# Performance work log

Measured on AMD Instinct MI355X. Metric: run time of the kernel, lower is better.

Reference implementation:

```python
import jax, jax.numpy as jnp
import numpy as np
import itertools

# ---- module constants (mirroring HyperLayer init) ----
B = 16          # batchsize
K = 16384       # number of learned index tuples (k)
ADD = 32        # additional sampled integer tuples per point
RANK = 2        # len(learn_cols) = w_rank; learn_cols = (0, 1)
P = 2 ** RANK + ADD  # candidate integer tuples per real-valued point
IN_DIM = 65536
OUT_DIM = 65536
EPSILON = 1e-6
SIGMA_BOOST = 2.0

# floor/ceil mask: rows of itertools.product([True, False], repeat=RANK) -> (2^RANK, RANK)
_FLOOR_MASK = jnp.array(
    [[int(b) for b in bools] for bools in itertools.product([True, False], repeat=RANK)],
    dtype=bool,
)


def setup_inputs() -> dict:
    key = jax.random.key(0)
    k1, k2, k3, k4 = jax.random.split(key, 4)
    return {
        "x": jax.random.normal(k1, (B, IN_DIM), jnp.float32),
        "res": jax.random.normal(k2, (B, K, RANK + 2), jnp.float32),
        "bias": jax.random.normal(k3, (OUT_DIM,), jnp.float32),
        "temp_indices": jax.random.randint(k4, (K, 2), 0, IN_DIM, dtype=jnp.int64),
    }


def _forward(x, res, bias, temp_indices):
    bsz = x.shape[0]
    # subrange = [out_size, in_size] for learn_cols = (0, 1)
    size = jnp.array([OUT_DIM, IN_DIM], jnp.float32)

    # ---- split_out: means in [0, size-1], sigmas softplus-scaled by size ----
    means = jax.nn.sigmoid(res[..., :RANK]) * (size - 1.0)               # (B, K, 2)
    sigmas = (jax.nn.softplus(res[..., RANK] + SIGMA_BOOST) + EPSILON)[..., None] * size  # (B, K, 2)
    values = res[..., RANK + 1]                                          # (B, K)

    # ---- discretize: 2^RANK floor/ceil neighbors (on detached means) ----
    m_det = jax.lax.stop_gradient(means)[:, :, None, :]                  # (B, K, 1, 2)
    nb = jnp.where(_FLOOR_MASK[None, None], jnp.floor(m_det), jnp.ceil(m_det)).astype(jnp.int32)  # (B,K,4,2)

    # additional uniformly sampled integer tuples (fixed internal key, deterministic)
    u = jax.random.uniform(jax.random.key(42), (bsz, K, ADD, RANK), jnp.float32) * (1.0 - EPSILON)
    samp = jnp.floor(u * size).astype(jnp.int32)                         # (B, K, ADD, 2)

    ints = jnp.concatenate([nb, samp], axis=2)                           # (B, K, P, 2)
    ints_fl = ints.astype(jnp.float32)

    # diagonal-Gaussian densities of integer tuples under (means, sigmas)
    z = (ints_fl - means[:, :, None, :]) / sigmas[:, :, None, :]         # (B, K, P, 2)
    props = jnp.exp(-0.5 * jnp.sum(z * z, axis=-1))                      # (B, K, P)
    props = props / jnp.sum(props + EPSILON, axis=2, keepdims=True)

    vals = (values[:, :, None] * props).reshape(bsz, -1)                 # (B, L)
    idx = ints.reshape(bsz, -1, RANK)                                    # (B, L, 2)

    # template: hardwired temp_indices, with learn_cols overwritten by discretized indices
    template = jnp.broadcast_to(
        temp_indices.astype(jnp.int32)[None, :, None, :], (bsz, K, P, 2)
    ).reshape(bsz, -1, 2)
    template = template.at[:, :, jnp.array([0, 1])].set(idx)

    out_idx = template[..., 0]                                           # (B, L) in [0, OUT_DIM)
    in_idx = template[..., 1]                                            # (B, L) in [0, IN_DIM)

    # sparse matrix-vector product per batch element: gather then scatter-add
    gathered = jnp.take_along_axis(x, in_idx, axis=1)                    # (B, L)
    contrib = vals * gathered                                            # (B, L)
    flat = (jnp.arange(bsz, dtype=jnp.int32)[:, None] * OUT_DIM + out_idx).reshape(-1)
    y = jnp.zeros((bsz * OUT_DIM,), x.dtype).at[flat].add(contrib.reshape(-1))
    return y.reshape(bsz, OUT_DIM) + bias[None, :]


def reference(x, res, bias, temp_indices):
    return _forward(x, res, bias, temp_indices)
```

## Files before the change

kernel.cpp:

```cpp
#include <hip/hip_runtime.h>
#include <stdint.h>
#include <math.h>

#define NB 16
#define NK 16384
#define NADD 32
#define NP 36
#define DIM 65536
#define NCH 4
#define CHW 16384
#define GPB 16

__device__ __forceinline__ uint32_t rotl32(uint32_t x, uint32_t r) {
    return (x << r) | (x >> (32u - r));
}

__device__ __forceinline__ uint32_t tf_bits(uint32_t idx) {
    const uint32_t K1 = 42u;
    const uint32_t K2 = 0x1BD11BDAu ^ 42u;
    uint32_t x0 = 0u;
    uint32_t x1 = idx + K1;
#define TF_ROUND(r) { x0 += x1; x1 = rotl32(x1, r); x1 ^= x0; }
#define TF_G(a,b,c,d) TF_ROUND(a) TF_ROUND(b) TF_ROUND(c) TF_ROUND(d)
    TF_G(13,15,26,6)   x0 += K1;  x1 += K2 + 1u;
    TF_G(17,29,16,24)  x0 += K2;  x1 += 2u;
    TF_G(13,15,26,6)              x1 += K1 + 3u;
    TF_G(17,29,16,24)  x0 += K1;  x1 += K2 + 4u;
    TF_G(13,15,26,6)   x0 += K2;  x1 += 5u;
#undef TF_G
#undef TF_ROUND
    return x0 ^ x1;
}

__device__ __forceinline__ float xla_expf(float x0) {
    float x = fminf(fmaxf(x0, -88.3762626647949f), 88.3762626647950f);
    const float fx = floorf(__fadd_rn(__fmul_rn(x, 1.44269504088896341f), 0.5f));
    const float tmp = __fmul_rn(fx, 0.693359375f);
    float z = __fmul_rn(fx, -2.12194440e-4f);
    float r = __fsub_rn(x, tmp);
    r = __fsub_rn(r, z);
    z = __fmul_rn(r, r);
    float y = 1.9875691500E-4f;
    y = __fadd_rn(__fmul_rn(y, r), 1.3981999507E-3f);
    y = __fadd_rn(__fmul_rn(y, r), 8.3334519073E-3f);
    y = __fadd_rn(__fmul_rn(y, r), 4.1665795894E-2f);
    y = __fadd_rn(__fmul_rn(y, r), 1.6666665459E-1f);
    y = __fadd_rn(__fmul_rn(y, r), 5.0000001201E-1f);
    y = __fadd_rn(__fmul_rn(y, z), r);
    y = __fadd_rn(y, 1.0f);
    const int n = (int)fx;
    const float p2n = __uint_as_float((uint32_t)(n + 127) << 23);
    return fmaxf(__fmul_rn(y, p2n), x0);
}

__device__ __forceinline__ void gen_point(const float4 r, uint32_t tid,
                                          uint32_t* packed, float* w) {
    const float e0 = xla_expf(-r.x);
    const float e1 = xla_expf(-r.y);
    const float s0 = __fdiv_rn(1.0f, __fadd_rn(1.0f, e0));
    const float s1 = __fdiv_rn(1.0f, __fadd_rn(1.0f, e1));
    const float m0 = __fmul_rn(s0, 65535.0f);
    const float m1 = __fmul_rn(s1, 65535.0f);

    const float a2 = r.z + 2.0f;
    const float sp = fmaxf(a2, 0.0f) + log1pf(expf(-fabsf(a2)));
    const float sigma = (sp + 1e-6f) * 65536.0f;
    const float val = r.w;

    const float f0 = floorf(m0), c0 = ceilf(m0);
    const float f1 = floorf(m1), c1 = ceilf(m1);
    {
        const float cd0[4] = {f0, f0, c0, c0};
        const float cd1[4] = {f1, c1, f1, c1};
        #pragma unroll
        for (int p = 0; p < 4; ++p) {
            const float z0 = (cd0[p] - m0) / sigma;
            const float z1 = (cd1[p] - m1) / sigma;
            w[p] = expf(-0.5f * (z0*z0 + z1*z1));
            packed[p] = ((uint32_t)(int)cd0[p] << 16) | (uint32_t)(int)cd1[p];
        }
    }
    const float ONE_MEPS = (float)(1.0 - 1e-6);
    const uint32_t base = tid * 64u;
    #pragma unroll
    for (int a = 0; a < NADD; ++a) {
        const uint32_t bb0 = tf_bits(base + 2u*(uint32_t)a);
        const uint32_t bb1 = tf_bits(base + 2u*(uint32_t)a + 1u);
        const float u0 = __fmul_rn(__uint_as_float((bb0 >> 9) | 0x3f800000u) - 1.0f, ONE_MEPS);
        const float u1 = __fmul_rn(__uint_as_float((bb1 >> 9) | 0x3f800000u) - 1.0f, ONE_MEPS);
        const float s0f = floorf(__fmul_rn(u0, 65536.0f));
        const float s1f = floorf(__fmul_rn(u1, 65536.0f));
        const float z0 = (s0f - m0) / sigma;
        const float z1 = (s1f - m1) / sigma;
        w[4 + a] = expf(-0.5f * (z0*z0 + z1*z1));
        packed[4 + a] = ((uint32_t)(int)s0f << 16) | (uint32_t)(int)s1f;
    }
    float denom = 0.0f;
    #pragma unroll
    for (int p = 0; p < NP; ++p) denom += w[p] + 1e-6f;
    const float scale = val / denom;
    #pragma unroll
    for (int p = 0; p < NP; ++p) w[p] *= scale;
}


__global__ __launch_bounds__(1024) void f1_gen_reduce(
    const float*  __restrict__ x,
    const float4* __restrict__ res4,
    float* __restrict__ part)
{
    __shared__ float acc[CHW];
    const int blk = blockIdx.x;
    const int b = blk >> 4;
    const uint32_t tid = (uint32_t)blk * 1024u + threadIdx.x;

    uint32_t packed[NP];
    float    w[NP];
    gen_point(res4[tid], tid, packed, w);

    const float* __restrict__ xrow = x + ((size_t)b << 16);
    #pragma unroll
    for (int p = 0; p < NP; ++p) w[p] *= xrow[packed[p] & 0xFFFFu];

    float* __restrict__ dst = part + ((size_t)blk << 16);
    #pragma unroll 1
    for (int c = 0; c < NCH; ++c) {
        for (int j = threadIdx.x; j < CHW; j += 1024) acc[j] = 0.0f;
        __syncthreads();
        #pragma unroll
        for (int p = 0; p < NP; ++p) {
            if ((packed[p] >> 30) == (uint32_t)c)
                atomicAdd(&acc[(packed[p] >> 16) & (CHW - 1)], w[p]);
        }
        __syncthreads();
        for (int j = threadIdx.x; j < CHW; j += 1024) dst[c * CHW + j] = acc[j];
        __syncthreads();
    }
}

__global__ __launch_bounds__(256) void f2_final(
    const float4* __restrict__ part4,
    const float4* __restrict__ bias4,
    float4* __restrict__ y4)
{
    const int i = blockIdx.x * 256 + threadIdx.x;
    const int o4 = i & 16383;
    const int b = i >> 14;
    float4 s = bias4[o4];
    #pragma unroll
    for (int g = 0; g < GPB; ++g) {
        const float4 p = part4[(((size_t)(b * GPB + g)) << 14) + o4];
        s.x += p.x; s.y += p.y; s.z += p.z; s.w += p.w;
    }
    y4[i] = s;
}


__global__ __launch_bounds__(256) void init_bias_kernel(
    const float4* __restrict__ bias4, float4* __restrict__ y4)
{
    const int i = blockIdx.x * 256 + threadIdx.x;
    y4[i] = bias4[i & 16383];
}

__global__ __launch_bounds__(256) void hyper_scatter(
    const float*  __restrict__ x,
    const float4* __restrict__ res4,
    float*        __restrict__ y)
{
    const int tid = blockIdx.x * 256 + threadIdx.x;
    const int b = tid >> 14;
    uint32_t packed[NP];
    float    w[NP];
    gen_point(res4[tid], (uint32_t)tid, packed, w);
    const float* __restrict__ xrow = x + ((size_t)b << 16);
    float*       __restrict__ yrow = y + ((size_t)b << 16);
    #pragma unroll
    for (int p = 0; p < NP; ++p) {
        const float xv = xrow[packed[p] & 0xFFFFu];
        unsafeAtomicAdd(&yrow[packed[p] >> 16], w[p] * xv);
    }
}

extern "C" void kernel_launch(void* const* d_in, const int* in_sizes, int n_in,
                              void* d_out, int out_size, void* d_ws, size_t ws_size,
                              hipStream_t stream) {
    const float*  x     = (const float*)d_in[0];
    const float4* res4  = (const float4*)d_in[1];
    const float4* bias4 = (const float4*)d_in[2];
    float* y = (float*)d_out;

    const size_t part_bytes = (size_t)NB * GPB * DIM * 4;

    if (ws_size >= part_bytes) {
        float* part = (float*)d_ws;
        f1_gen_reduce<<<NB * GPB, 1024, 0, stream>>>(x, res4, part);
        f2_final<<<(NB * DIM / 4) / 256, 256, 0, stream>>>((const float4*)part, bias4, (float4*)y);
    } else {
        init_bias_kernel<<<(NB * DIM / 4) / 256, 256, 0, stream>>>(bias4, (float4*)y);
        hyper_scatter<<<(NB * NK) / 256, 256, 0, stream>>>(x, res4, y);
    }
}
```

Before: 178.2 us.

## Replace partial-buffer reduction with shared-memory binning plus sparse global atomics

Each block still bins its points' contributions in shared memory, now using 512 threads and 8 chunks of 8192 outputs. Instead of writing a dense partial buffer per block and summing those in a second kernel, each block atomically adds only its nonzero bin entries straight into the output, which is first set to the bias. This removes the large partial-buffer write and read-back. The cost is more global atomic traffic, more chunk passes and barriers per block, and summation order that varies between runs.

```diff
diff --git a/kernel.cpp b/kernel.cpp
--- a/kernel.cpp
+++ b/kernel.cpp
@@ -7,9 +7,12 @@
 #define NADD 32
 #define NP 36
 #define DIM 65536
-#define NCH 4
-#define CHW 16384
-#define GPB 16
+
+#define TPB 512
+#define NCH2 8
+#define CHW2 8192
+
+typedef float f32x4 __attribute__((ext_vector_type(4)));
 
 __device__ __forceinline__ uint32_t rotl32(uint32_t x, uint32_t r) {
     return (x << r) | (x >> (32u - r));
@@ -103,16 +106,23 @@
     for (int p = 0; p < NP; ++p) w[p] *= scale;
 }
 
+__global__ __launch_bounds__(256) void init_bias_kernel(
+    const float4* __restrict__ bias4, float4* __restrict__ y4)
+{
+    const int i = blockIdx.x * 256 + threadIdx.x;
+    y4[i] = bias4[i & 16383];
+}
 
-__global__ __launch_bounds__(1024) void f1_gen_reduce(
+__global__ __launch_bounds__(TPB, 4) void f1_gen_atomic(
     const float*  __restrict__ x,
     const float4* __restrict__ res4,
-    float* __restrict__ part)
+    float* __restrict__ y)
 {
-    __shared__ float acc[CHW];
+    __shared__ float acc[CHW2];
+    f32x4* const acc4 = reinterpret_cast<f32x4*>(acc);
     const int blk = blockIdx.x;
-    const int b = blk >> 4;
-    const uint32_t tid = (uint32_t)blk * 1024u + threadIdx.x;
+    const uint32_t tid = (uint32_t)blk * TPB + threadIdx.x;
+    const int b = (int)(tid >> 14);
 
     uint32_t packed[NP];
     float    w[NP];
@@ -120,48 +130,35 @@
 
     const float* __restrict__ xrow = x + ((size_t)b << 16);
     #pragma unroll
-    for (int p = 0; p < NP; ++p) w[p] *= xrow[packed[p] & 0xFFFFu];
+    for (int p = 0; p < NP; ++p) {
+        w[p] *= xrow[packed[p] & 0xFFFFu];
+        packed[p] = packed[p] >> 16;
+    }
 
-    float* __restrict__ dst = part + ((size_t)blk << 16);
+    float* __restrict__ yrow = y + ((size_t)b << 16);
     #pragma unroll 1
-    for (int c = 0; c < NCH; ++c) {
-        for (int j = threadIdx.x; j < CHW; j += 1024) acc[j] = 0.0f;
+    for (uint32_t c = 0; c < NCH2; ++c) {
+        #pragma unroll
+        for (int j = 0; j < 4; ++j)
+            acc4[j * TPB + threadIdx.x] = (f32x4)(0.0f);
         __syncthreads();
         #pragma unroll
         for (int p = 0; p < NP; ++p) {
-            if ((packed[p] >> 30) == (uint32_t)c)
-                atomicAdd(&acc[(packed[p] >> 16) & (CHW - 1)], w[p]);
+            if ((packed[p] >> 13) == c)
+                atomicAdd(&acc[packed[p] & (CHW2 - 1)], w[p]);
         }
         __syncthreads();
-        for (int j = threadIdx.x; j < CHW; j += 1024) dst[c * CHW + j] = acc[j];
+        float* __restrict__ ydst = yrow + c * CHW2;
+        #pragma unroll
+        for (int j = 0; j < 16; ++j) {
+            const int idx = j * TPB + (int)threadIdx.x;
+            const float v = acc[idx];
+            if (v != 0.0f) unsafeAtomicAdd(&ydst[idx], v);
+        }
         __syncthreads();
     }
 }
 
-__global__ __launch_bounds__(256) void f2_final(
-    const float4* __restrict__ part4,
-    const float4* __restrict__ bias4,
-    float4* __restrict__ y4)
-{
-    const int i = blockIdx.x * 256 + threadIdx.x;
-    const int o4 = i & 16383;
-    const int b = i >> 14;
-    float4 s = bias4[o4];
-    #pragma unroll
-    for (int g = 0; g < GPB; ++g) {
-        const float4 p = part4[(((size_t)(b * GPB + g)) << 14) + o4];
-        s.x += p.x; s.y += p.y; s.z += p.z; s.w += p.w;
-    }
-    y4[i] = s;
-}
-
-
-__global__ __launch_bounds__(256) void init_bias_kernel(
-    const float4* __restrict__ bias4, float4* __restrict__ y4)
-{
-    const int i = blockIdx.x * 256 + threadIdx.x;
-    y4[i] = bias4[i & 16383];
-}
 
 __global__ __launch_bounds__(256) void hyper_scatter(
     const float*  __restrict__ x,
@@ -190,14 +187,8 @@
     const float4* bias4 = (const float4*)d_in[2];
     float* y = (float*)d_out;
 
-    const size_t part_bytes = (size_t)NB * GPB * DIM * 4;
+    (void)d_ws; (void)ws_size;
 
-    if (ws_size >= part_bytes) {
-        float* part = (float*)d_ws;
-        f1_gen_reduce<<<NB * GPB, 1024, 0, stream>>>(x, res4, part);
-        f2_final<<<(NB * DIM / 4) / 256, 256, 0, stream>>>((const float4*)part, bias4, (float4*)y);
-    } else {
-        init_bias_kernel<<<(NB * DIM / 4) / 256, 256, 0, stream>>>(bias4, (float4*)y);
-        hyper_scatter<<<(NB * NK) / 256, 256, 0, stream>>>(x, res4, y);
-    }
+    init_bias_kernel<<<(NB * DIM / 4) / 256, 256, 0, stream>>>(bias4, (float4*)y);
+    f1_gen_atomic<<<NB * NK / TPB, TPB, 0, stream>>>(x, res4, y);
 }
```

Result: slower. 208.0 us (+16.7%).
